# Performance work log

Hardware: AMD Instinct MI355X
Metric: run time of the kernel (lower is better)

Reference implementation:

```python
import jax, jax.numpy as jnp
import numpy as np

MARGIN = 0.2  # init kwarg
_EPS = 1e-12


def _pairwise_dist(x):
    # Euclidean cdist via the Gram trick; safe sqrt so grads stay finite at d=0.
    sq = jnp.sum(x * x, axis=1)
    d2 = sq[:, None] + sq[None, :] - 2.0 * (x @ x.T)
    d2 = jnp.maximum(d2, 0.0)
    safe = jnp.where(d2 > _EPS, d2, _EPS)
    return jnp.where(d2 > _EPS, jnp.sqrt(safe), 0.0)


def setup_inputs() -> dict:
    key = jax.random.key(0)
    k1, k2 = jax.random.split(key)
    B, D = 8192, 128
    embeddings = jax.random.normal(k1, (B, D), dtype=jnp.float32)
    labels = jax.random.randint(k2, (B,), 0, 64)
    return {"embeddings": embeddings, "labels": labels}


def reference(embeddings, labels):
    B = embeddings.shape[0]
    d = _pairwise_dist(embeddings)                      # [B, B]
    eq = labels[None, :] == labels[:, None]             # [B, B] bool (incl. diag)
    pos_mask = eq.astype(d.dtype) - jnp.eye(B, dtype=d.dtype)  # positives, no self
    hardest_positive = jnp.max(d * pos_mask, axis=1)    # [B]
    max_dist = jnp.max(d)
    # push non-negatives (same label, incl. self) out of the min
    hardest_negative = jnp.min(d + max_dist * eq.astype(d.dtype), axis=1)  # [B]
    losses = jax.nn.relu(hardest_positive - hardest_negative + MARGIN)
    return jnp.mean(losses)
```

## Files before the change

### kernel.cpp

```cpp
#include <hip/hip_runtime.h>
#include <hip/hip_bf16.h>


#define BB 8192
#define DD 128
#define MARGIN 0.2f
#define EPS 1e-12f

#define GCOLS 16
#define COLS_PER_WAVE 512
#define NGROUPS (COLS_PER_WAVE / GCOLS)

typedef __attribute__((ext_vector_type(8))) short short8;
typedef __attribute__((ext_vector_type(4))) float f32x4;

__device__ inline unsigned short f2bf(float f) {
    __hip_bfloat16 h = __float2bfloat16(f);
    unsigned short u;
    __builtin_memcpy(&u, &h, 2);
    return u;
}

__global__ __launch_bounds__(256) void prep_kernel(
    const float* __restrict__ x, const int* __restrict__ lab,
    unsigned short* __restrict__ xb, float2* __restrict__ meta,
    unsigned* __restrict__ hp2, unsigned* __restrict__ mn2,
    unsigned long long* __restrict__ fsum, unsigned* __restrict__ fdone) {
    int t = blockIdx.x * blockDim.x + threadIdx.x;
    int row = t >> 5;
    const float4 v = reinterpret_cast<const float4*>(x)[t];

    union { unsigned short u[4]; uint2 w; } p;
    p.u[0] = f2bf(v.x); p.u[1] = f2bf(v.y);
    p.u[2] = f2bf(v.z); p.u[3] = f2bf(v.w);
    reinterpret_cast<uint2*>(xb)[t] = p.w;

    float s = v.x * v.x + v.y * v.y + v.z * v.z + v.w * v.w;
    #pragma unroll
    for (int m = 16; m >= 1; m >>= 1) s += __shfl_xor(s, m, 64);
    if ((t & 31) == 0) meta[row] = make_float2(s, __int_as_float(lab[row]));

    if (t < BB) { hp2[t] = 0u; mn2[t] = 0x7f800000u; }
    if (t == 0) { *fsum = 0ull; *fdone = 0u; }
}

__global__ __launch_bounds__(256) void triplet_main(
    const unsigned short* __restrict__ xb, const float2* __restrict__ meta,
    unsigned* __restrict__ hp2, unsigned* __restrict__ mn2) {
    const int tid  = threadIdx.x;
    const int wave = tid >> 6;
    const int lane = tid & 63;
    const int l15  = lane & 15;
    const int lhi  = lane >> 4;

    const int cc    = blockIdx.x & 15;
    const int rw    = (blockIdx.x >> 4) * 4 + wave;
    const int rbase = rw * 32;
    const int cbase = cc * COLS_PER_WAVE;

    __shared__ unsigned short sbuf[4][2][GCOLS * DD];
    __shared__ float2 smeta[COLS_PER_WAVE];

    short8 a0[4], a1[4];
    {
        const unsigned short* ar0 = xb + (size_t)(rbase + l15) * DD + lhi * 8;
        const unsigned short* ar1 = ar0 + 16 * DD;
        #pragma unroll
        for (int s = 0; s < 4; ++s) {
            a0[s] = *reinterpret_cast<const short8*>(ar0 + s * 32);
            a1[s] = *reinterpret_cast<const short8*>(ar1 + s * 32);
        }
    }
    unsigned li0 = 0, li1 = 0;
    #pragma unroll
    for (int k = 0; k < 4; ++k) {
        li0 |= ((unsigned)__float_as_int(meta[rbase + lhi * 4 + k].y) & 255u) << (8 * k);
        li1 |= ((unsigned)__float_as_int(meta[rbase + 16 + lhi * 4 + k].y) & 255u) << (8 * k);
    }
    float hp0[4], mn0[4], hp1[4], mn1[4];
    #pragma unroll
    for (int k = 0; k < 4; ++k) {
        hp0[k] = -__builtin_inff(); mn0[k] = __builtin_inff();
        hp1[k] = -__builtin_inff(); mn1[k] = __builtin_inff();
    }

    auto stage = [&](int g) {
        const char* sb_ = (const char*)(xb + (size_t)(cbase + g * GCOLS) * DD);
        char* db = (char*)&sbuf[wave][g & 1][0];
        #pragma unroll
        for (int p = 0; p < 4; ++p) {
            const int o     = p * 1024 + lane * 16;
            const int col   = o >> 8;
            const int inner = (o & 255) ^ ((col & 7) << 4);
            __builtin_amdgcn_global_load_lds(
                (const __attribute__((address_space(1))) void*)(sb_ + col * 256 + inner),
                (__attribute__((address_space(3))) void*)(db + p * 1024), 16, 0, 0);
        }
    };

    auto body = [&](int g, bool do_stage) {
        const char* bb_ = (const char*)&sbuf[wave][g & 1][0];
        short8 b[4];
        #pragma unroll
        for (int s = 0; s < 4; ++s)
            b[s] = *reinterpret_cast<const short8*>(
                bb_ + l15 * 256 + ((s * 64 + lhi * 16) ^ ((l15 & 7) << 4)));
        const float2 cm = *reinterpret_cast<const float2*>(
            (const char*)smeta + ((size_t)g * 16 + l15) * 8);
        asm volatile("s_waitcnt lgkmcnt(0)" ::: "memory");
        __builtin_amdgcn_sched_barrier(0);
        if (do_stage) stage(g + 2);
        f32x4 acc0 = {}, acc1 = {};
        #pragma unroll
        for (int s = 0; s < 4; ++s) {
            acc0 = __builtin_amdgcn_mfma_f32_16x16x32_bf16(a0[s], b[s], acc0, 0, 0, 0);
            acc1 = __builtin_amdgcn_mfma_f32_16x16x32_bf16(a1[s], b[s], acc1, 0, 0, 0);
        }
        const float sqj = cm.x;
        const int   labj = __float_as_int(cm.y) & 255;
        #pragma unroll
        for (int k = 0; k < 4; ++k) {
            const float d0 = fmaf(acc0[k], -2.0f, sqj);
            const float d1 = fmaf(acc1[k], -2.0f, sqj);
            const bool e0 = (int)((li0 >> (8 * k)) & 255u) == labj;
            const bool e1 = (int)((li1 >> (8 * k)) & 255u) == labj;
            hp0[k] = fmaxf(hp0[k], e0 ? d0 : -__builtin_inff());
            mn0[k] = fminf(mn0[k], e0 ? __builtin_inff() : d0);
            hp1[k] = fmaxf(hp1[k], e1 ? d1 : -__builtin_inff());
            mn1[k] = fminf(mn1[k], e1 ? __builtin_inff() : d1);
        }
    };

    {
        const char* msrc = (const char*)(meta + cbase);
        #pragma unroll
        for (int p = 0; p < 4; ++p)
            __builtin_amdgcn_global_load_lds(
                (const __attribute__((address_space(1))) void*)(msrc + p * 1024 + lane * 16),
                (__attribute__((address_space(3))) void*)((char*)smeta + p * 1024), 16, 0, 0);
    }
    stage(0);
    stage(1);

    for (int g = 0; g < NGROUPS - 2; ++g) {
        asm volatile("s_waitcnt vmcnt(4)" ::: "memory");
        body(g, true);
    }
    asm volatile("s_waitcnt vmcnt(4)" ::: "memory");
    body(NGROUPS - 2, false);
    asm volatile("s_waitcnt vmcnt(0)" ::: "memory");
    body(NGROUPS - 1, false);

    #pragma unroll
    for (int k = 0; k < 4; ++k) {
        const float sqi0 = meta[rbase + lhi * 4 + k].x;
        const float sqi1 = meta[rbase + 16 + lhi * 4 + k].x;
        hp0[k] = fmaxf(sqi0 + hp0[k], 0.0f);  mn0[k] = sqi0 + mn0[k];
        hp1[k] = fmaxf(sqi1 + hp1[k], 0.0f);  mn1[k] = sqi1 + mn1[k];
    }
    #pragma unroll
    for (int m = 1; m < 16; m <<= 1) {
        #pragma unroll
        for (int k = 0; k < 4; ++k) {
            hp0[k] = fmaxf(hp0[k], __shfl_xor(hp0[k], m, 64));
            mn0[k] = fminf(mn0[k], __shfl_xor(mn0[k], m, 64));
            hp1[k] = fmaxf(hp1[k], __shfl_xor(hp1[k], m, 64));
            mn1[k] = fminf(mn1[k], __shfl_xor(mn1[k], m, 64));
        }
    }
    if (l15 == 0) {
        #pragma unroll
        for (int k = 0; k < 4; ++k) {
            const int i0 = rbase + lhi * 4 + k;
            const int i1 = i0 + 16;
            atomicMax(&hp2[i0], __float_as_uint(hp0[k]));
            atomicMin(&mn2[i0], __float_as_uint(mn0[k]));
            atomicMax(&hp2[i1], __float_as_uint(hp1[k]));
            atomicMin(&mn2[i1], __float_as_uint(mn1[k]));
        }
    }
}

__device__ inline float d_of(float d2) {
    return (d2 > EPS) ? sqrtf(d2) : 0.0f;
}

__global__ __launch_bounds__(1024) void finalize_kernel(
    const unsigned* __restrict__ hp2, const unsigned* __restrict__ mn2,
    unsigned long long* __restrict__ fsum, unsigned* __restrict__ fdone,
    float* __restrict__ out) {
    const int i = blockIdx.x * 1024 + threadIdx.x;
    const float hpv = d_of(__uint_as_float(hp2[i]));
    const float mnv = d_of(__uint_as_float(mn2[i]));
    float acc = fmaxf(hpv - mnv + MARGIN, 0.0f);

    #pragma unroll
    for (int m = 1; m < 64; m <<= 1) acc += __shfl_xor(acc, m, 64);
    __shared__ float ws[16];
    const int wave = threadIdx.x >> 6;
    if ((threadIdx.x & 63) == 0) ws[wave] = acc;
    __syncthreads();
    if (threadIdx.x == 0) {
        float s = 0.0f;
        #pragma unroll
        for (int w = 0; w < 16; ++w) s += ws[w];
        atomicAdd(fsum, (unsigned long long)((double)s * 4294967296.0));
        __threadfence();
        const unsigned old = atomicAdd(fdone, 1u);
        if (old == gridDim.x - 1) {
            const unsigned long long total = atomicAdd(fsum, 0ull);
            out[0] = (float)((double)total / 4294967296.0 / (double)BB);
        }
    }
}

extern "C" void kernel_launch(void* const* d_in, const int* in_sizes, int n_in,
                              void* d_out, int out_size, void* d_ws, size_t ws_size,
                              hipStream_t stream) {
    const float* x = (const float*)d_in[0];
    const int* lab = (const int*)d_in[1];
    float* out = (float*)d_out;

    char* ws = (char*)d_ws;
    unsigned short* xb = (unsigned short*)ws;
    float2* meta = (float2*)(ws + (size_t)BB * DD * 2);
    unsigned* hp2 = (unsigned*)(ws + (size_t)BB * DD * 2 + BB * 8);
    unsigned* mn2 = (unsigned*)(ws + (size_t)BB * DD * 2 + BB * 12);
    unsigned long long* fsum = (unsigned long long*)(ws + (size_t)BB * DD * 2 + BB * 16);
    unsigned* fdone = (unsigned*)(ws + (size_t)BB * DD * 2 + BB * 16 + 8);

    prep_kernel<<<(BB * DD / 4) / 256, 256, 0, stream>>>(x, lab, xb, meta, hp2, mn2, fsum, fdone);
    triplet_main<<<1024, 256, 0, stream>>>(xb, meta, hp2, mn2);
    finalize_kernel<<<BB / 1024, 1024, 0, stream>>>(hp2, mn2, fsum, fdone, out);
}
```

Measured before the change: 47.49 us.

## Sort rows by label so tiles take uniform positive/negative fast paths

Adds a counting sort of rows by label (histogram, scan, scatter, permuted bf16 copy) before the main kernel. Each wave's 32-row tile then usually holds one label, so column groups wholly outside or inside that label's range update only the min or only the max, with no per-element label compare. It also widens the LDS swizzle to 16 columns. In exchange it adds four small kernel launches, atomics, and a scattered write pass, which may cost more than the select work saved in a kernel that is already short.

```diff
diff --git a/kernel.cpp b/kernel.cpp
--- a/kernel.cpp
+++ b/kernel.cpp
@@ -21,32 +21,74 @@
     return u;
 }
 
-__global__ __launch_bounds__(256) void prep_kernel(
+__global__ __launch_bounds__(256) void init_small(
+    unsigned* __restrict__ hist, unsigned* __restrict__ cnt,
+    unsigned long long* __restrict__ fsum, unsigned* __restrict__ fdone) {
+    const int t = threadIdx.x;
+    if (t < 64) { hist[t] = 0u; cnt[t] = 0u; }
+    if (t == 0) { *fsum = 0ull; *fdone = 0u; }
+}
+
+__global__ __launch_bounds__(256) void prep_meta(
     const float* __restrict__ x, const int* __restrict__ lab,
-    unsigned short* __restrict__ xb, float2* __restrict__ meta,
-    unsigned* __restrict__ hp2, unsigned* __restrict__ mn2,
-    unsigned long long* __restrict__ fsum, unsigned* __restrict__ fdone) {
-    int t = blockIdx.x * blockDim.x + threadIdx.x;
-    int row = t >> 5;
+    float2* __restrict__ meta, unsigned* __restrict__ hist,
+    unsigned* __restrict__ hp2, unsigned* __restrict__ mn2) {
+    const int t = blockIdx.x * 256 + threadIdx.x;
+    const int row = t >> 5;
     const float4 v = reinterpret_cast<const float4*>(x)[t];
-
-    union { unsigned short u[4]; uint2 w; } p;
-    p.u[0] = f2bf(v.x); p.u[1] = f2bf(v.y);
-    p.u[2] = f2bf(v.z); p.u[3] = f2bf(v.w);
-    reinterpret_cast<uint2*>(xb)[t] = p.w;
-
     float s = v.x * v.x + v.y * v.y + v.z * v.z + v.w * v.w;
     #pragma unroll
     for (int m = 16; m >= 1; m >>= 1) s += __shfl_xor(s, m, 64);
-    if ((t & 31) == 0) meta[row] = make_float2(s, __int_as_float(lab[row]));
-
+    if ((t & 31) == 0) {
+        const int l = lab[row];
+        meta[row] = make_float2(s, __int_as_float(l));
+        atomicAdd(&hist[l], 1u);
+    }
     if (t < BB) { hp2[t] = 0u; mn2[t] = 0x7f800000u; }
-    if (t == 0) { *fsum = 0ull; *fdone = 0u; }
+}
+
+__global__ __launch_bounds__(64) void scan64(
+    const unsigned* __restrict__ hist, int* __restrict__ labstart) {
+    const int l = threadIdx.x;
+    unsigned v = hist[l];
+    #pragma unroll
+    for (int off = 1; off < 64; off <<= 1) {
+        const unsigned n = __shfl_up(v, off, 64);
+        if (l >= off) v += n;
+    }
+    labstart[l + 1] = (int)v;
+    if (l == 0) labstart[0] = 0;
+}
+
+__global__ __launch_bounds__(256) void scatter_idx(
+    const float2* __restrict__ meta, const int* __restrict__ labstart,
+    unsigned* __restrict__ cnt, int* __restrict__ prow,
+    float2* __restrict__ meta_s) {
+    const int r = blockIdx.x * 256 + threadIdx.x;
+    const float2 m = meta[r];
+    const int l = __float_as_int(m.y);
+    const int p = labstart[l] + (int)atomicAdd(&cnt[l], 1u);
+    prow[r] = p;
+    meta_s[p] = m;
+}
+
+__global__ __launch_bounds__(256) void copy_sorted(
+    const float* __restrict__ x, const int* __restrict__ prow,
+    unsigned short* __restrict__ xs) {
+    const int t = blockIdx.x * 256 + threadIdx.x;
+    const int row = t >> 5;
+    const int p = prow[row];
+    const float4 v = reinterpret_cast<const float4*>(x)[t];
+    union { unsigned short u[4]; uint2 w; } pk;
+    pk.u[0] = f2bf(v.x); pk.u[1] = f2bf(v.y);
+    pk.u[2] = f2bf(v.z); pk.u[3] = f2bf(v.w);
+    reinterpret_cast<uint2*>(xs)[p * 32 + (t & 31)] = pk.w;
 }
 
 __global__ __launch_bounds__(256) void triplet_main(
-    const unsigned short* __restrict__ xb, const float2* __restrict__ meta,
-    unsigned* __restrict__ hp2, unsigned* __restrict__ mn2) {
+    const unsigned short* __restrict__ xs, const float2* __restrict__ meta_s,
+    const int* __restrict__ labstart, unsigned* __restrict__ hp2,
+    unsigned* __restrict__ mn2) {
     const int tid  = threadIdx.x;
     const int wave = tid >> 6;
     const int lane = tid & 63;
@@ -63,7 +105,7 @@
 
     short8 a0[4], a1[4];
     {
-        const unsigned short* ar0 = xb + (size_t)(rbase + l15) * DD + lhi * 8;
+        const unsigned short* ar0 = xs + (size_t)(rbase + l15) * DD + lhi * 8;
         const unsigned short* ar1 = ar0 + 16 * DD;
         #pragma unroll
         for (int s = 0; s < 4; ++s) {
@@ -71,11 +113,17 @@
             a1[s] = *reinterpret_cast<const short8*>(ar1 + s * 32);
         }
     }
+    const int L0  = __builtin_amdgcn_readfirstlane(__float_as_int(meta_s[rbase].y));
+    const int L31 = __builtin_amdgcn_readfirstlane(__float_as_int(meta_s[rbase + 31].y));
+    const int ps  = labstart[L0];
+    const int pe  = labstart[L0 + 1];
+    const bool uni = (L0 == L31);
+
     unsigned li0 = 0, li1 = 0;
     #pragma unroll
     for (int k = 0; k < 4; ++k) {
-        li0 |= ((unsigned)__float_as_int(meta[rbase + lhi * 4 + k].y) & 255u) << (8 * k);
-        li1 |= ((unsigned)__float_as_int(meta[rbase + 16 + lhi * 4 + k].y) & 255u) << (8 * k);
+        li0 |= ((unsigned)__float_as_int(meta_s[rbase + lhi * 4 + k].y) & 255u) << (8 * k);
+        li1 |= ((unsigned)__float_as_int(meta_s[rbase + 16 + lhi * 4 + k].y) & 255u) << (8 * k);
     }
     float hp0[4], mn0[4], hp1[4], mn1[4];
     #pragma unroll
@@ -85,13 +133,13 @@
     }
 
     auto stage = [&](int g) {
-        const char* sb_ = (const char*)(xb + (size_t)(cbase + g * GCOLS) * DD);
+        const char* sb_ = (const char*)(xs + (size_t)(cbase + g * GCOLS) * DD);
         char* db = (char*)&sbuf[wave][g & 1][0];
         #pragma unroll
         for (int p = 0; p < 4; ++p) {
             const int o     = p * 1024 + lane * 16;
             const int col   = o >> 8;
-            const int inner = (o & 255) ^ ((col & 7) << 4);
+            const int inner = (o & 255) ^ ((col & 15) << 4);
             __builtin_amdgcn_global_load_lds(
                 (const __attribute__((address_space(1))) void*)(sb_ + col * 256 + inner),
                 (__attribute__((address_space(3))) void*)(db + p * 1024), 16, 0, 0);
@@ -104,9 +152,8 @@
         #pragma unroll
         for (int s = 0; s < 4; ++s)
             b[s] = *reinterpret_cast<const short8*>(
-                bb_ + l15 * 256 + ((s * 64 + lhi * 16) ^ ((l15 & 7) << 4)));
-        const float2 cm = *reinterpret_cast<const float2*>(
-            (const char*)smeta + ((size_t)g * 16 + l15) * 8);
+                bb_ + l15 * 256 + ((s * 64 + lhi * 16) ^ (l15 << 4)));
+        const float2 cm = smeta[g * GCOLS + l15];
         asm volatile("s_waitcnt lgkmcnt(0)" ::: "memory");
         __builtin_amdgcn_sched_barrier(0);
         if (do_stage) stage(g + 2);
@@ -117,22 +164,50 @@
             acc1 = __builtin_amdgcn_mfma_f32_16x16x32_bf16(a1[s], b[s], acc1, 0, 0, 0);
         }
         const float sqj = cm.x;
-        const int   labj = __float_as_int(cm.y) & 255;
-        #pragma unroll
-        for (int k = 0; k < 4; ++k) {
-            const float d0 = fmaf(acc0[k], -2.0f, sqj);
-            const float d1 = fmaf(acc1[k], -2.0f, sqj);
-            const bool e0 = (int)((li0 >> (8 * k)) & 255u) == labj;
-            const bool e1 = (int)((li1 >> (8 * k)) & 255u) == labj;
-            hp0[k] = fmaxf(hp0[k], e0 ? d0 : -__builtin_inff());
-            mn0[k] = fminf(mn0[k], e0 ? __builtin_inff() : d0);
-            hp1[k] = fmaxf(hp1[k], e1 ? d1 : -__builtin_inff());
-            mn1[k] = fminf(mn1[k], e1 ? __builtin_inff() : d1);
+        const int c0 = cbase + g * GCOLS;
+        if (uni) {
+            if (c0 >= pe || c0 + GCOLS <= ps) {
+                #pragma unroll
+                for (int k = 0; k < 4; ++k) {
+                    mn0[k] = fminf(mn0[k], fmaf(acc0[k], -2.0f, sqj));
+                    mn1[k] = fminf(mn1[k], fmaf(acc1[k], -2.0f, sqj));
+                }
+            } else if (c0 >= ps && c0 + GCOLS <= pe) {
+                #pragma unroll
+                for (int k = 0; k < 4; ++k) {
+                    hp0[k] = fmaxf(hp0[k], fmaf(acc0[k], -2.0f, sqj));
+                    hp1[k] = fmaxf(hp1[k], fmaf(acc1[k], -2.0f, sqj));
+                }
+            } else {
+                const bool eq = (__float_as_int(cm.y) == L0);
+                #pragma unroll
+                for (int k = 0; k < 4; ++k) {
+                    const float d0 = fmaf(acc0[k], -2.0f, sqj);
+                    const float d1 = fmaf(acc1[k], -2.0f, sqj);
+                    hp0[k] = fmaxf(hp0[k], eq ? d0 : -__builtin_inff());
+                    mn0[k] = fminf(mn0[k], eq ? __builtin_inff() : d0);
+                    hp1[k] = fmaxf(hp1[k], eq ? d1 : -__builtin_inff());
+                    mn1[k] = fminf(mn1[k], eq ? __builtin_inff() : d1);
+                }
+            }
+        } else {
+            const int labj = __float_as_int(cm.y) & 255;
+            #pragma unroll
+            for (int k = 0; k < 4; ++k) {
+                const float d0 = fmaf(acc0[k], -2.0f, sqj);
+                const float d1 = fmaf(acc1[k], -2.0f, sqj);
+                const bool e0k = (int)((li0 >> (8 * k)) & 255u) == labj;
+                const bool e1k = (int)((li1 >> (8 * k)) & 255u) == labj;
+                hp0[k] = fmaxf(hp0[k], e0k ? d0 : -__builtin_inff());
+                mn0[k] = fminf(mn0[k], e0k ? __builtin_inff() : d0);
+                hp1[k] = fmaxf(hp1[k], e1k ? d1 : -__builtin_inff());
+                mn1[k] = fminf(mn1[k], e1k ? __builtin_inff() : d1);
+            }
         }
     };
 
     {
-        const char* msrc = (const char*)(meta + cbase);
+        const char* msrc = (const char*)(meta_s + cbase);
         #pragma unroll
         for (int p = 0; p < 4; ++p)
             __builtin_amdgcn_global_load_lds(
@@ -141,7 +216,6 @@
     }
     stage(0);
     stage(1);
-
     for (int g = 0; g < NGROUPS - 2; ++g) {
         asm volatile("s_waitcnt vmcnt(4)" ::: "memory");
         body(g, true);
@@ -153,8 +227,8 @@
 
     #pragma unroll
     for (int k = 0; k < 4; ++k) {
-        const float sqi0 = meta[rbase + lhi * 4 + k].x;
-        const float sqi1 = meta[rbase + 16 + lhi * 4 + k].x;
+        const float sqi0 = meta_s[rbase + lhi * 4 + k].x;
+        const float sqi1 = meta_s[rbase + 16 + lhi * 4 + k].x;
         hp0[k] = fmaxf(sqi0 + hp0[k], 0.0f);  mn0[k] = sqi0 + mn0[k];
         hp1[k] = fmaxf(sqi1 + hp1[k], 0.0f);  mn1[k] = sqi1 + mn1[k];
     }
@@ -222,14 +296,24 @@
     float* out = (float*)d_out;
 
     char* ws = (char*)d_ws;
-    unsigned short* xb = (unsigned short*)ws;
-    float2* meta = (float2*)(ws + (size_t)BB * DD * 2);
-    unsigned* hp2 = (unsigned*)(ws + (size_t)BB * DD * 2 + BB * 8);
-    unsigned* mn2 = (unsigned*)(ws + (size_t)BB * DD * 2 + BB * 12);
-    unsigned long long* fsum = (unsigned long long*)(ws + (size_t)BB * DD * 2 + BB * 16);
-    unsigned* fdone = (unsigned*)(ws + (size_t)BB * DD * 2 + BB * 16 + 8);
-
-    prep_kernel<<<(BB * DD / 4) / 256, 256, 0, stream>>>(x, lab, xb, meta, hp2, mn2, fsum, fdone);
-    triplet_main<<<1024, 256, 0, stream>>>(xb, meta, hp2, mn2);
+    unsigned short* xs = (unsigned short*)ws;
+    size_t off = (size_t)BB * DD * 2;
+    float2* meta   = (float2*)(ws + off);  off += (size_t)BB * 8;
+    float2* meta_s = (float2*)(ws + off);  off += (size_t)BB * 8;
+    unsigned* hp2  = (unsigned*)(ws + off); off += (size_t)BB * 4;
+    unsigned* mn2  = (unsigned*)(ws + off); off += (size_t)BB * 4;
+    int* prow      = (int*)(ws + off);      off += (size_t)BB * 4;
+    unsigned* hist = (unsigned*)(ws + off); off += 64 * 4;
+    unsigned* cnt  = (unsigned*)(ws + off); off += 64 * 4;
+    int* labstart  = (int*)(ws + off);      off += 65 * 4;
+    unsigned long long* fsum = (unsigned long long*)(ws + ((off + 7) & ~(size_t)7));
+    unsigned* fdone = (unsigned*)((char*)fsum + 8);
+
+    init_small<<<1, 256, 0, stream>>>(hist, cnt, fsum, fdone);
+    prep_meta<<<(BB * 32) / 256, 256, 0, stream>>>(x, lab, meta, hist, hp2, mn2);
+    scan64<<<1, 64, 0, stream>>>(hist, labstart);
+    scatter_idx<<<BB / 256, 256, 0, stream>>>(meta, labstart, cnt, prow, meta_s);
+    copy_sorted<<<(BB * 32) / 256, 256, 0, stream>>>(x, prow, xs);
+    triplet_main<<<1024, 256, 0, stream>>>(xs, meta_s, labstart, hp2, mn2);
     finalize_kernel<<<BB / 1024, 1024, 0, stream>>>(hp2, mn2, fsum, fdone, out);
 }
```

New measurement: 102.8 us (median of 2 runs). 116% more time.

## Share column tiles across eight waves with a block-wide triple-buffered pipeline

Applied to the files above, without the earlier changes.

The main kernel now uses 512-thread blocks on a 2D grid. Each block covers 256 rows by 256 columns. Column tiles of 32 embeddings are staged once into shared LDS buffers and reused by all eight waves, where before each wave streamed its own private tiles. A three-buffer ring with block-wide barriers replaces the per-wave double buffer. This cuts redundant global/L2 traffic for column data, at the cost of s_barrier synchronization each stage and more blocks, each doing a shorter inner loop.

```diff
diff --git a/kernel.cpp b/kernel.cpp
--- a/kernel.cpp
+++ b/kernel.cpp
@@ -7,9 +7,11 @@
 #define MARGIN 0.2f
 #define EPS 1e-12f
 
-#define GCOLS 16
-#define COLS_PER_WAVE 512
-#define NGROUPS (COLS_PER_WAVE / GCOLS)
+#define COLS_PER_BLOCK 256
+#define ROWS_PER_BLOCK 256
+#define STAGE_COLS 32
+#define NSTAGES 8
+#define STAGE_SHORTS (STAGE_COLS * DD)
 
 typedef __attribute__((ext_vector_type(8))) short short8;
 typedef __attribute__((ext_vector_type(4))) float f32x4;
@@ -44,7 +46,7 @@
     if (t == 0) { *fsum = 0ull; *fdone = 0u; }
 }
 
-__global__ __launch_bounds__(256) void triplet_main(
+__global__ __launch_bounds__(512) void triplet_main(
     const unsigned short* __restrict__ xb, const float2* __restrict__ meta,
     unsigned* __restrict__ hp2, unsigned* __restrict__ mn2) {
     const int tid  = threadIdx.x;
@@ -52,14 +54,11 @@
     const int lane = tid & 63;
     const int l15  = lane & 15;
     const int lhi  = lane >> 4;
-
-    const int cc    = blockIdx.x & 15;
-    const int rw    = (blockIdx.x >> 4) * 4 + wave;
-    const int rbase = rw * 32;
-    const int cbase = cc * COLS_PER_WAVE;
-
-    __shared__ unsigned short sbuf[4][2][GCOLS * DD];
-    __shared__ float2 smeta[COLS_PER_WAVE];
+    const int rbase = blockIdx.x * ROWS_PER_BLOCK + wave * 32;
+    const int cbase = blockIdx.y * COLS_PER_BLOCK;
+
+    __shared__ unsigned short sb[3][STAGE_SHORTS];
+    __shared__ float2 smeta[COLS_PER_BLOCK];
 
     short8 a0[4], a1[4];
     {
@@ -84,40 +83,36 @@
         hp1[k] = -__builtin_inff(); mn1[k] = __builtin_inff();
     }
 
-    auto stage = [&](int g) {
-        const char* sb_ = (const char*)(xb + (size_t)(cbase + g * GCOLS) * DD);
-        char* db = (char*)&sbuf[wave][g & 1][0];
-        #pragma unroll
-        for (int p = 0; p < 4; ++p) {
-            const int o     = p * 1024 + lane * 16;
-            const int col   = o >> 8;
-            const int inner = (o & 255) ^ ((col & 7) << 4);
-            __builtin_amdgcn_global_load_lds(
-                (const __attribute__((address_space(1))) void*)(sb_ + col * 256 + inner),
-                (__attribute__((address_space(3))) void*)(db + p * 1024), 16, 0, 0);
-        }
+    auto stage = [&](int g, int buf) {
+        const char* src_base = (const char*)(xb + (size_t)(cbase + g * STAGE_COLS) * DD);
+        const int o   = tid * 16;
+        const int row = o >> 8;
+        const int byt = (o & 255) ^ ((row & 15) << 4);
+        const char* src = src_base + row * 256 + byt;
+        char* dst = (char*)&sb[buf][0] + wave * 1024;
+        __builtin_amdgcn_global_load_lds(
+            (const __attribute__((address_space(1))) void*)src,
+            (__attribute__((address_space(3))) void*)dst, 16, 0, 0);
     };
 
-    auto body = [&](int g, bool do_stage) {
-        const char* bb_ = (const char*)&sbuf[wave][g & 1][0];
+    auto compute_group = [&](int st, int gg, const char* base) {
+        const int jl = gg * 16 + l15;
+        const int rowoff = jl * 256;
+        const int swz = (jl & 15) << 4;
         short8 b[4];
         #pragma unroll
         for (int s = 0; s < 4; ++s)
             b[s] = *reinterpret_cast<const short8*>(
-                bb_ + l15 * 256 + ((s * 64 + lhi * 16) ^ ((l15 & 7) << 4)));
-        const float2 cm = *reinterpret_cast<const float2*>(
-            (const char*)smeta + ((size_t)g * 16 + l15) * 8);
-        asm volatile("s_waitcnt lgkmcnt(0)" ::: "memory");
-        __builtin_amdgcn_sched_barrier(0);
-        if (do_stage) stage(g + 2);
+                base + rowoff + ((s * 64 + lhi * 16) ^ swz));
         f32x4 acc0 = {}, acc1 = {};
         #pragma unroll
         for (int s = 0; s < 4; ++s) {
             acc0 = __builtin_amdgcn_mfma_f32_16x16x32_bf16(a0[s], b[s], acc0, 0, 0, 0);
             acc1 = __builtin_amdgcn_mfma_f32_16x16x32_bf16(a1[s], b[s], acc1, 0, 0, 0);
         }
-        const float sqj = cm.x;
-        const int   labj = __float_as_int(cm.y) & 255;
+        const float2 mj = smeta[st * STAGE_COLS + jl];
+        const float sqj = mj.x;
+        const int   labj = __float_as_int(mj.y) & 255;
         #pragma unroll
         for (int k = 0; k < 4; ++k) {
             const float d0 = fmaf(acc0[k], -2.0f, sqj);
@@ -134,22 +129,28 @@
     {
         const char* msrc = (const char*)(meta + cbase);
         #pragma unroll
-        for (int p = 0; p < 4; ++p)
+        for (int p = 0; p < 2; ++p)
             __builtin_amdgcn_global_load_lds(
                 (const __attribute__((address_space(1))) void*)(msrc + p * 1024 + lane * 16),
                 (__attribute__((address_space(3))) void*)((char*)smeta + p * 1024), 16, 0, 0);
     }
-    stage(0);
-    stage(1);
-
-    for (int g = 0; g < NGROUPS - 2; ++g) {
-        asm volatile("s_waitcnt vmcnt(4)" ::: "memory");
-        body(g, true);
-    }
-    asm volatile("s_waitcnt vmcnt(4)" ::: "memory");
-    body(NGROUPS - 2, false);
-    asm volatile("s_waitcnt vmcnt(0)" ::: "memory");
-    body(NGROUPS - 1, false);
+    stage(0, 0);
+    stage(1, 1);
+
+    #pragma unroll
+    for (int st = 0; st < NSTAGES; ++st) {
+        if (st < NSTAGES - 1)
+            asm volatile("s_waitcnt lgkmcnt(0) vmcnt(1)" ::: "memory");
+        else
+            asm volatile("s_waitcnt lgkmcnt(0) vmcnt(0)" ::: "memory");
+        __builtin_amdgcn_s_barrier();
+        __builtin_amdgcn_sched_barrier(0);
+        if (st + 2 < NSTAGES) stage(st + 2, (st + 2) % 3);
+        const char* base = (const char*)&sb[st % 3][0];
+        compute_group(st, 0, base);
+        __builtin_amdgcn_sched_barrier(0);
+        compute_group(st, 1, base);
+    }
 
     #pragma unroll
     for (int k = 0; k < 4; ++k) {
@@ -230,6 +231,7 @@
     unsigned* fdone = (unsigned*)(ws + (size_t)BB * DD * 2 + BB * 16 + 8);
 
     prep_kernel<<<(BB * DD / 4) / 256, 256, 0, stream>>>(x, lab, xb, meta, hp2, mn2, fsum, fdone);
-    triplet_main<<<1024, 256, 0, stream>>>(xb, meta, hp2, mn2);
+    dim3 grid(BB / ROWS_PER_BLOCK, BB / COLS_PER_BLOCK);
+    triplet_main<<<grid, 512, 0, stream>>>(xb, meta, hp2, mn2);
     finalize_kernel<<<BB / 1024, 1024, 0, stream>>>(hp2, mn2, fsum, fdone, out);
 }
```

New measurement: 43.15 us. -9.2%, faster.

## Halve columns per wave, single-buffer LDS, double grid size

Applied to the files above, without the earlier changes.

Each block now covers 256 columns instead of 512, and the grid doubles to 2048 blocks. The block index is remapped so consecutive blocks share a column chunk. The LDS B tile drops from double to single buffering, which halves shared memory per block and may allow more resident blocks. The prefetch distance shrinks to one group with a full vmcnt(0) wait, the XOR swizzle changes to a 16-way pattern, and the loop is fully unrolled. The aim is more parallelism and occupancy, at the cost of less load/compute overlap within a wave and twice as many atomic row-reduction writes.

```diff
diff --git a/kernel.cpp b/kernel.cpp
--- a/kernel.cpp
+++ b/kernel.cpp
@@ -8,8 +8,8 @@
 #define EPS 1e-12f
 
 #define GCOLS 16
-#define COLS_PER_WAVE 512
-#define NGROUPS (COLS_PER_WAVE / GCOLS)
+#define COLS_PER_WAVE 256
+#define NGROUPS 16
 
 typedef __attribute__((ext_vector_type(8))) short short8;
 typedef __attribute__((ext_vector_type(4))) float f32x4;
@@ -53,12 +53,12 @@
     const int l15  = lane & 15;
     const int lhi  = lane >> 4;
 
-    const int cc    = blockIdx.x & 15;
-    const int rw    = (blockIdx.x >> 4) * 4 + wave;
+    const int cc    = blockIdx.x >> 6;
+    const int rw    = (blockIdx.x & 63) * 4 + wave;
     const int rbase = rw * 32;
     const int cbase = cc * COLS_PER_WAVE;
 
-    __shared__ unsigned short sbuf[4][2][GCOLS * DD];
+    __shared__ unsigned short sbuf[4][GCOLS * DD];
     __shared__ float2 smeta[COLS_PER_WAVE];
 
     short8 a0[4], a1[4];
@@ -86,12 +86,11 @@
 
     auto stage = [&](int g) {
         const char* sb_ = (const char*)(xb + (size_t)(cbase + g * GCOLS) * DD);
-        char* db = (char*)&sbuf[wave][g & 1][0];
+        char* db = (char*)&sbuf[wave][0];
         #pragma unroll
         for (int p = 0; p < 4; ++p) {
-            const int o     = p * 1024 + lane * 16;
-            const int col   = o >> 8;
-            const int inner = (o & 255) ^ ((col & 7) << 4);
+            const int col   = p * 4 + lhi;
+            const int inner = ((l15 ^ (col & 15)) << 4);
             __builtin_amdgcn_global_load_lds(
                 (const __attribute__((address_space(1))) void*)(sb_ + col * 256 + inner),
                 (__attribute__((address_space(3))) void*)(db + p * 1024), 16, 0, 0);
@@ -99,17 +98,16 @@
     };
 
     auto body = [&](int g, bool do_stage) {
-        const char* bb_ = (const char*)&sbuf[wave][g & 1][0];
+        const char* bb_ = (const char*)&sbuf[wave][0];
         short8 b[4];
         #pragma unroll
         for (int s = 0; s < 4; ++s)
             b[s] = *reinterpret_cast<const short8*>(
-                bb_ + l15 * 256 + ((s * 64 + lhi * 16) ^ ((l15 & 7) << 4)));
-        const float2 cm = *reinterpret_cast<const float2*>(
-            (const char*)smeta + ((size_t)g * 16 + l15) * 8);
+                bb_ + l15 * 256 + ((s * 64 + lhi * 16) ^ (l15 << 4)));
+        const float2 cm = smeta[g * GCOLS + l15];
         asm volatile("s_waitcnt lgkmcnt(0)" ::: "memory");
         __builtin_amdgcn_sched_barrier(0);
-        if (do_stage) stage(g + 2);
+        if (do_stage) stage(g + 1);
         f32x4 acc0 = {}, acc1 = {};
         #pragma unroll
         for (int s = 0; s < 4; ++s) {
@@ -134,22 +132,17 @@
     {
         const char* msrc = (const char*)(meta + cbase);
         #pragma unroll
-        for (int p = 0; p < 4; ++p)
+        for (int p = 0; p < 2; ++p)
             __builtin_amdgcn_global_load_lds(
                 (const __attribute__((address_space(1))) void*)(msrc + p * 1024 + lane * 16),
                 (__attribute__((address_space(3))) void*)((char*)smeta + p * 1024), 16, 0, 0);
     }
     stage(0);
-    stage(1);
-
-    for (int g = 0; g < NGROUPS - 2; ++g) {
-        asm volatile("s_waitcnt vmcnt(4)" ::: "memory");
-        body(g, true);
-    }
-    asm volatile("s_waitcnt vmcnt(4)" ::: "memory");
-    body(NGROUPS - 2, false);
-    asm volatile("s_waitcnt vmcnt(0)" ::: "memory");
-    body(NGROUPS - 1, false);
+    #pragma unroll
+    for (int g = 0; g < NGROUPS; ++g) {
+        asm volatile("s_waitcnt vmcnt(0)" ::: "memory");
+        body(g, g + 1 < NGROUPS);
+    }
 
     #pragma unroll
     for (int k = 0; k < 4; ++k) {
@@ -230,6 +223,6 @@
     unsigned* fdone = (unsigned*)(ws + (size_t)BB * DD * 2 + BB * 16 + 8);
 
     prep_kernel<<<(BB * DD / 4) / 256, 256, 0, stream>>>(x, lab, xb, meta, hp2, mn2, fsum, fdone);
-    triplet_main<<<1024, 256, 0, stream>>>(xb, meta, hp2, mn2);
+    triplet_main<<<2048, 256, 0, stream>>>(xb, meta, hp2, mn2);
     finalize_kernel<<<BB / 1024, 1024, 0, stream>>>(hp2, mn2, fsum, fdone, out);
 }
```

Result: slower. 51.44 us (+8.3%).
